# Optimization experiments

Hardware: AMD Instinct MI355X
Metric: run time of the kernel (lower is better)

Reference implementation:

```python
import jax, jax.numpy as jnp
import numpy as np

jax.config.update("jax_enable_x64", True)

# Module hyperparameters (from init_kwargs)
NUM_EMB = 1_000_000
EMB_DIM = 128
COMPRESSION = 1.0 / 64.0
WEIGHT_SIZE = int(NUM_EMB * EMB_DIM * COMPRESSION)  # 2_000_000 (1D compressed table)

# Hash constants matching the CUDA kernel's multiplicative hash:
# hashed_idx = (index * P1 + dim * P2) mod weight_size
P1 = np.uint64(9824516537)
P2 = np.uint64(57857966300227)

BATCH = 16384
BAG_LEN = 50


def _hashed_idx(indices):
    # indices: [N] int -> hashed positions [N, EMB_DIM] into the 1D weight table
    flat = indices.reshape(-1).astype(jnp.uint64)
    dims = jnp.arange(EMB_DIM, dtype=jnp.uint64)
    h = (flat[:, None] * P1 + dims[None, :] * P2) % jnp.uint64(WEIGHT_SIZE)
    return h.astype(jnp.int64)


def setup_inputs() -> dict:
    key = jax.random.key(0)
    k1, k2 = jax.random.split(key)
    indices = jax.random.randint(k1, (BATCH, BAG_LEN), 0, NUM_EMB, dtype=jnp.int64)
    # reset_parameters(): init.normal_(weight)
    weight = jax.random.normal(k2, (WEIGHT_SIZE,), dtype=jnp.float32)
    return {"weight": weight, "indices": indices}


def reference(weight, indices):
    # 2D indices path: each row is one bag of fixed length; mode='sum'.
    B, L = indices.shape
    hidx = _hashed_idx(indices)                      # [B*L, D]
    emb = weight[hidx].reshape(B, L, EMB_DIM)        # gather from compressed table
    return emb.sum(axis=1)                           # [B, D] per-bag sum
```

## Files before the change

kernel.cpp:

```cpp
#include <hip/hip_runtime.h>
#include <stdint.h>


#define WS       2000000
#define EMB_DIM  128
#define BAG_LEN  50
#define BATCH    16384

#define NBLK     256
#define NTHR     1024
#define BAGS_PB  64
#define NQUAD    16
#define QEXT     408
#define RSZE     65536
#define NREG     31
#define SBIG     300227u
#define SENT     0x10000000u

#define GLOAD_LDS16(gp, lp)                                            \
    __builtin_amdgcn_global_load_lds(                                  \
        (const __attribute__((address_space(1))) uint32_t*)(gp),       \
        (__attribute__((address_space(3))) uint32_t*)(lp), 16, 0, 0)

__global__ __launch_bounds__(1024) void conv_bf16(
    const float* __restrict__ w, uint16_t* __restrict__ o)
{
    const int i = (blockIdx.x * 1024 + threadIdx.x) * 4;
    if (i >= WS) return;
    const float4 f = *(const float4*)(w + i);
    uint32_t u0 = __float_as_uint(f.x), u1 = __float_as_uint(f.y);
    uint32_t u2 = __float_as_uint(f.z), u3 = __float_as_uint(f.w);
    ushort4 r;
    r.x = (uint16_t)((u0 + 0x7FFFu + ((u0 >> 16) & 1u)) >> 16);
    r.y = (uint16_t)((u1 + 0x7FFFu + ((u1 >> 16) & 1u)) >> 16);
    r.z = (uint16_t)((u2 + 0x7FFFu + ((u2 >> 16) & 1u)) >> 16);
    r.w = (uint16_t)((u3 + 0x7FFFu + ((u3 >> 16) & 1u)) >> 16);
    *(ushort4*)(o + i) = r;
}

__global__ __launch_bounds__(NTHR, 4) void heb_bf16(
    const uint16_t* __restrict__ wbf,
    const int*      __restrict__ indices,
    float*          __restrict__ out)
{
    __shared__ __align__(16) uint16_t tile[RSZE];
    __shared__ uint32_t extq[NQUAD][QEXT];

    const int tid     = threadIdx.x;
    const int d       = tid & 127;
    const int g       = tid >> 7;
    const int bagBase = blockIdx.x * BAGS_PB;

    uint32_t* araw = (uint32_t*)&tile[0];
    uint32_t* S    = (uint32_t*)&tile[0] + 4096;

    for (int p = tid; p < NQUAD * QEXT; p += NTHR)
        ((uint32_t*)extq)[p] = SENT;
    for (int p = tid; p < BAGS_PB * BAG_LEN; p += NTHR) {
        uint32_t b = (uint32_t)p / 50u;
        uint32_t i = (uint32_t)p - b * 50u;
        uint64_t idx = (uint64_t)(uint32_t)indices[bagBase * BAG_LEN + p];
        araw[b * 52 + i] = (uint32_t)((idx * 9824516537ull) % (uint64_t)WS);
    }
    __syncthreads();

    for (int p = tid; p < BAGS_PB * BAG_LEN; p += NTHR) {
        uint32_t b = (uint32_t)p / 50u;
        uint32_t i = (uint32_t)p - b * 50u;
        uint32_t v = araw[b * 52 + i];
        int rank = 0;
        for (int q = 0; q < BAG_LEN; ++q) {
            uint32_t w = araw[b * 52 + q];
            rank += (w < v || (w == v && q < (int)i)) ? 1 : 0;
        }
        S[b * 52 + rank] = v;
    }
    __syncthreads();

    for (int p = tid; p < BAGS_PB * BAG_LEN; p += NTHR) {
        uint32_t bag = (uint32_t)p / 50u;
        uint32_t i   = (uint32_t)p - bag * 50u;
        uint32_t qd  = bag >> 2, b = bag & 3u;
        uint32_t v = S[bag * 52 + i];
        int r = (int)i;
        for (uint32_t b2 = 0; b2 < 4u; ++b2) {
            if (b2 == b) continue;
            const uint32_t* T = &S[((qd << 2) + b2) * 52];
            uint32_t key = (b2 < b) ? v + 1u : v;
            int lo = 0, hi = 50;
            while (lo < hi) {
                int mid = (lo + hi) >> 1;
                bool lt = T[mid] < key;
                lo = lt ? mid + 1 : lo;
                hi = lt ? hi : mid;
            }
            r += lo;
        }
        extq[qd][r]       = (v << 2) | b;
        extq[qd][r + 200] = ((v + (uint32_t)WS) << 2) | b;
    }
    __syncthreads();

    const uint32_t c  = ((uint32_t)d * SBIG) % (uint32_t)WS;
    const uint32_t C4 = (uint32_t)(((int)c - WS) * 4);
    const uint32_t limit = ((uint32_t)WS - c) << 2;

    uint32_t t4[2], K[2];
    float sm[2][4];
#pragma unroll
    for (int qi = 0; qi < 2; ++qi) {
        const uint32_t* eg = &extq[(g << 1) + qi][0];
        int lo = 0, hi = 200;
        while (lo < hi) {
            int mid = (lo + hi) >> 1;
            bool lt = eg[mid] < limit;
            lo = lt ? mid + 1 : lo;
            hi = lt ? hi : mid;
        }
        t4[qi] = (uint32_t)lo << 2;
        K[qi]  = eg[lo];
        sm[qi][0] = sm[qi][1] = sm[qi][2] = sm[qi][3] = 0.0f;
    }

    for (int r = 0; r < NREG; ++r) {
        const int lo  = r * RSZE;
        const int len = (RSZE < WS - lo) ? RSZE : (WS - lo);
        __syncthreads();

        for (int s = tid; s < (len >> 3); s += NTHR)
            GLOAD_LDS16(wbf + lo + (s << 3), &tile[s << 3]);
        __syncthreads();

        const uint32_t len4 = (uint32_t)len << 2;
        const uint32_t CL   = C4 - (((uint32_t)lo) << 2);
        const char* tb = (const char*)&tile[0];

#pragma unroll
        for (int qi = 0; qi < 2; ++qi) {
            const char* eg = (const char*)&extq[(g << 1) + qi][0];
            uint32_t t_ = t4[qi], K_ = K[qi];
            uint32_t u  = K_ + CL;
            float s0 = sm[qi][0], s1 = sm[qi][1];
            float s2 = sm[qi][2], s3 = sm[qi][3];
            while (u < len4) {
                const uint32_t raw =
                    *(const uint16_t*)(tb + ((u >> 1) & ~1u));
                const float v = __uint_as_float(raw << 16);
                const uint32_t tag = u & 3u;
                s0 += (tag == 0u) ? v : 0.0f;
                s1 += (tag == 1u) ? v : 0.0f;
                s2 += (tag == 2u) ? v : 0.0f;
                s3 += (tag == 3u) ? v : 0.0f;
                t_ += 4u;
                K_  = *(const uint32_t*)(eg + t_);
                u   = K_ + CL;
            }
            t4[qi] = t_; K[qi] = K_;
            sm[qi][0] = s0; sm[qi][1] = s1; sm[qi][2] = s2; sm[qi][3] = s3;
        }
    }

#pragma unroll
    for (int qi = 0; qi < 2; ++qi)
#pragma unroll
        for (int b = 0; b < 4; ++b) {
            const int bag = (g << 3) + (qi << 2) + b;
            out[(size_t)(bagBase + bag) * EMB_DIM + d] = sm[qi][b];
        }
}

#define RSIZE_FB 32768
#define NREG_FB  62
#define EXT_N    104
#define SENT4    0x10000000u

__global__ __launch_bounds__(NTHR, 4) void heb_single(
    const float* __restrict__ weight,
    const int*   __restrict__ indices,
    float*       __restrict__ out)
{
    __shared__ __align__(16) float tile[RSIZE_FB];
    __shared__ uint32_t ext4[BAGS_PB][EXT_N];
    const int tid = threadIdx.x, d = tid & 127, bag_lo = tid >> 7;
    const int bagBase = blockIdx.x * BAGS_PB;
    uint32_t* araw = (uint32_t*)&tile[0];
    for (int p = tid; p < BAGS_PB * BAG_LEN; p += NTHR) {
        uint32_t g = (uint32_t)p / 50u, i = (uint32_t)p - g * 50u;
        uint64_t idx = (uint64_t)(uint32_t)indices[bagBase * BAG_LEN + p];
        araw[g * 52 + i] = (uint32_t)((idx * 9824516537ull) % (uint64_t)WS);
    }
    __syncthreads();
    for (int p = tid; p < BAGS_PB * BAG_LEN; p += NTHR) {
        uint32_t g = (uint32_t)p / 50u, i = (uint32_t)p - g * 50u;
        uint32_t v = araw[g * 52 + i];
        int rank = 0;
        for (int q = 0; q < BAG_LEN; ++q) {
            uint32_t w = araw[g * 52 + q];
            rank += (w < v || (w == v && q < (int)i)) ? 1 : 0;
        }
        ext4[g][rank] = v << 2;
        ext4[g][rank + 50] = (v + (uint32_t)WS) << 2;
    }
    for (int p = tid; p < BAGS_PB * 4; p += NTHR)
        ext4[p >> 2][100 + (p & 3)] = SENT4;
    __syncthreads();
    const uint32_t c = ((uint32_t)d * SBIG) % (uint32_t)WS;
    const uint32_t C4 = (uint32_t)(((int)c - WS) * 4);
    const uint32_t wmc4 = ((uint32_t)WS - c) << 2;
    uint32_t t4[8], h4[8]; float sm[8];
#pragma unroll
    for (int k = 0; k < 8; ++k) {
        const uint32_t* eg = &ext4[(bag_lo << 3) + k][0];
        int nlow = 0;
        for (int q = 0; q < BAG_LEN; ++q) nlow += (eg[q] < wmc4) ? 1 : 0;
        t4[k] = (uint32_t)nlow << 2; h4[k] = eg[nlow] + C4; sm[k] = 0.0f;
    }
    for (int r = 0; r < NREG_FB; ++r) {
        const int lo = r * RSIZE_FB;
        const int len = (RSIZE_FB < WS - lo) ? RSIZE_FB : (WS - lo);
        __syncthreads();
        for (int s = tid; s < (len >> 2); s += NTHR)
            GLOAD_LDS16(weight + lo + (s << 2), &tile[s << 2]);
        __syncthreads();
        const uint32_t lo4 = ((uint32_t)lo) << 2;
        const uint32_t hi4 = (r == NREG_FB - 1) ? (uint32_t)(4 * WS)
                                                : lo4 + ((uint32_t)RSIZE_FB << 2);
        const char* tb = (const char*)&tile[0];
#pragma unroll
        for (int k = 0; k < 8; ++k) {
            const char* eg = (const char*)&ext4[(bag_lo << 3) + k][0];
            uint32_t t_ = t4[k], h_ = h4[k]; float s_ = sm[k];
            while (h_ < hi4) {
                s_ += *(const float*)(tb + (h_ - lo4));
                t_ += 4u;
                h_ = *(const uint32_t*)(eg + t_) + C4;
            }
            t4[k] = t_; h4[k] = h_; sm[k] = s_;
        }
    }
#pragma unroll
    for (int k = 0; k < 8; ++k)
        out[(size_t)(bagBase + (bag_lo << 3) + k) * EMB_DIM + d] = sm[k];
}

extern "C" void kernel_launch(void* const* d_in, const int* in_sizes, int n_in,
                              void* d_out, int out_size, void* d_ws, size_t ws_size,
                              hipStream_t stream)
{
    const float* weight  = (const float*)d_in[0];
    const int*   indices = (const int*)d_in[1];
    float*       out     = (float*)d_out;

    if (ws_size >= (size_t)WS * sizeof(uint16_t)) {
        uint16_t* wbf = (uint16_t*)d_ws;
        conv_bf16<<<(WS / 4 + 1023) / 1024, 1024, 0, stream>>>(weight, wbf);
        heb_bf16<<<NBLK, NTHR, 0, stream>>>(wbf, indices, out);
    } else {
        heb_single<<<NBLK, NTHR, 0, stream>>>(weight, indices, out);
    }
}
```

Before: 227.6 us.

## Merge 8 bags per thread stream and accumulate via LDS atomics

Each thread now walks a single merged sorted list covering 8 bags instead of two 4-bag lists. It accumulates into a shared-memory accumulator with atomicAdd rather than predicated register sums. The LDS tile shrinks to make room for the accumulator, so the number of weight-table regions grows, and the bf16 conversion kernel now processes 8 elements per thread. The aim is to drop the per-element 4-way select-add and the double loop overhead, at the cost of LDS atomics, more region passes and extra barriers.

```diff
diff --git a/kernel.cpp b/kernel.cpp
--- a/kernel.cpp
+++ b/kernel.cpp
@@ -10,41 +10,45 @@
 #define NBLK     256
 #define NTHR     1024
 #define BAGS_PB  64
-#define NQUAD    16
-#define QEXT     408
-#define RSZE     65536
-#define NREG     31
+#define TSZ      49152
+#define NREG     41
 #define SBIG     300227u
-#define SENT     0x10000000u
+#define EXT8_N   808
+#define SENT     0x7FFFFFFFu
 
 #define GLOAD_LDS16(gp, lp)                                            \
     __builtin_amdgcn_global_load_lds(                                  \
         (const __attribute__((address_space(1))) uint32_t*)(gp),       \
         (__attribute__((address_space(3))) uint32_t*)(lp), 16, 0, 0)
 
+__device__ __forceinline__ uint32_t f2bf(float x) {
+    uint32_t u = __float_as_uint(x);
+    return (u + 0x7FFFu + ((u >> 16) & 1u)) >> 16;
+}
+
 __global__ __launch_bounds__(1024) void conv_bf16(
     const float* __restrict__ w, uint16_t* __restrict__ o)
 {
-    const int i = (blockIdx.x * 1024 + threadIdx.x) * 4;
+    const int i = (blockIdx.x * 1024 + threadIdx.x) * 8;
     if (i >= WS) return;
-    const float4 f = *(const float4*)(w + i);
-    uint32_t u0 = __float_as_uint(f.x), u1 = __float_as_uint(f.y);
-    uint32_t u2 = __float_as_uint(f.z), u3 = __float_as_uint(f.w);
-    ushort4 r;
-    r.x = (uint16_t)((u0 + 0x7FFFu + ((u0 >> 16) & 1u)) >> 16);
-    r.y = (uint16_t)((u1 + 0x7FFFu + ((u1 >> 16) & 1u)) >> 16);
-    r.z = (uint16_t)((u2 + 0x7FFFu + ((u2 >> 16) & 1u)) >> 16);
-    r.w = (uint16_t)((u3 + 0x7FFFu + ((u3 >> 16) & 1u)) >> 16);
-    *(ushort4*)(o + i) = r;
-}
-
-__global__ __launch_bounds__(NTHR, 4) void heb_bf16(
+    const float4 f0 = *(const float4*)(w + i);
+    const float4 f1 = *(const float4*)(w + i + 4);
+    uint4 st;
+    st.x = f2bf(f0.x) | (f2bf(f0.y) << 16);
+    st.y = f2bf(f0.z) | (f2bf(f0.w) << 16);
+    st.z = f2bf(f1.x) | (f2bf(f1.y) << 16);
+    st.w = f2bf(f1.z) | (f2bf(f1.w) << 16);
+    *(uint4*)(o + i) = st;
+}
+
+__global__ __launch_bounds__(NTHR, 4) void heb_bf16v2(
     const uint16_t* __restrict__ wbf,
     const int*      __restrict__ indices,
     float*          __restrict__ out)
 {
-    __shared__ __align__(16) uint16_t tile[RSZE];
-    __shared__ uint32_t extq[NQUAD][QEXT];
+    __shared__ __align__(16) uint16_t tile[TSZ];
+    __shared__ float    acc[BAGS_PB * EMB_DIM];
+    __shared__ uint32_t ext8[8][EXT8_N];
 
     const int tid     = threadIdx.x;
     const int d       = tid & 127;
@@ -54,8 +58,9 @@
     uint32_t* araw = (uint32_t*)&tile[0];
     uint32_t* S    = (uint32_t*)&tile[0] + 4096;
 
-    for (int p = tid; p < NQUAD * QEXT; p += NTHR)
-        ((uint32_t*)extq)[p] = SENT;
+    for (int p = tid; p < BAGS_PB * EMB_DIM; p += NTHR) acc[p] = 0.0f;
+    for (int p = tid; p < 8 * EXT8_N; p += NTHR)
+        ((uint32_t*)ext8)[p] = SENT;
     for (int p = tid; p < BAGS_PB * BAG_LEN; p += NTHR) {
         uint32_t b = (uint32_t)p / 50u;
         uint32_t i = (uint32_t)p - b * 50u;
@@ -80,12 +85,12 @@
     for (int p = tid; p < BAGS_PB * BAG_LEN; p += NTHR) {
         uint32_t bag = (uint32_t)p / 50u;
         uint32_t i   = (uint32_t)p - bag * 50u;
-        uint32_t qd  = bag >> 2, b = bag & 3u;
+        uint32_t gg  = bag >> 3, b = bag & 7u;
         uint32_t v = S[bag * 52 + i];
         int r = (int)i;
-        for (uint32_t b2 = 0; b2 < 4u; ++b2) {
+        for (uint32_t b2 = 0; b2 < 8u; ++b2) {
             if (b2 == b) continue;
-            const uint32_t* T = &S[((qd << 2) + b2) * 52];
+            const uint32_t* T = &S[((gg << 3) + b2) * 52];
             uint32_t key = (b2 < b) ? v + 1u : v;
             int lo = 0, hi = 50;
             while (lo < hi) {
@@ -96,77 +101,57 @@
             }
             r += lo;
         }
-        extq[qd][r]       = (v << 2) | b;
-        extq[qd][r + 200] = ((v + (uint32_t)WS) << 2) | b;
+        ext8[gg][r]       = (v << 3) | b;
+        ext8[gg][r + 400] = ((v + (uint32_t)WS) << 3) | b;
     }
     __syncthreads();
 
     const uint32_t c  = ((uint32_t)d * SBIG) % (uint32_t)WS;
-    const uint32_t C4 = (uint32_t)(((int)c - WS) * 4);
-    const uint32_t limit = ((uint32_t)WS - c) << 2;
-
-    uint32_t t4[2], K[2];
-    float sm[2][4];
-#pragma unroll
-    for (int qi = 0; qi < 2; ++qi) {
-        const uint32_t* eg = &extq[(g << 1) + qi][0];
-        int lo = 0, hi = 200;
-        while (lo < hi) {
-            int mid = (lo + hi) >> 1;
-            bool lt = eg[mid] < limit;
-            lo = lt ? mid + 1 : lo;
-            hi = lt ? hi : mid;
-        }
-        t4[qi] = (uint32_t)lo << 2;
-        K[qi]  = eg[lo];
-        sm[qi][0] = sm[qi][1] = sm[qi][2] = sm[qi][3] = 0.0f;
-    }
+    const uint32_t C8 = (uint32_t)(((int)c - WS) * 8);
+    const uint32_t limit = ((uint32_t)WS - c) << 3;
+
+    const uint32_t* eg = &ext8[g][0];
+    int lo_ = 0, hi_ = 400;
+    while (lo_ < hi_) {
+        int mid = (lo_ + hi_) >> 1;
+        bool lt = eg[mid] < limit;
+        lo_ = lt ? mid + 1 : lo_;
+        hi_ = lt ? hi_ : mid;
+    }
+    uint32_t t_ = (uint32_t)lo_ << 2;
+    uint32_t K_ = eg[lo_];
+
+    const char* eb = (const char*)&ext8[g][0];
+    float* accG = acc + (g << 10) + d;
 
     for (int r = 0; r < NREG; ++r) {
-        const int lo  = r * RSZE;
-        const int len = (RSZE < WS - lo) ? RSZE : (WS - lo);
+        const int lo  = r * TSZ;
+        const int len = (TSZ < WS - lo) ? TSZ : (WS - lo);
         __syncthreads();
 
         for (int s = tid; s < (len >> 3); s += NTHR)
             GLOAD_LDS16(wbf + lo + (s << 3), &tile[s << 3]);
         __syncthreads();
 
-        const uint32_t len4 = (uint32_t)len << 2;
-        const uint32_t CL   = C4 - (((uint32_t)lo) << 2);
+        const uint32_t len8 = (uint32_t)len << 3;
+        const uint32_t CL   = C8 - (((uint32_t)lo) << 3);
         const char* tb = (const char*)&tile[0];
 
-#pragma unroll
-        for (int qi = 0; qi < 2; ++qi) {
-            const char* eg = (const char*)&extq[(g << 1) + qi][0];
-            uint32_t t_ = t4[qi], K_ = K[qi];
-            uint32_t u  = K_ + CL;
-            float s0 = sm[qi][0], s1 = sm[qi][1];
-            float s2 = sm[qi][2], s3 = sm[qi][3];
-            while (u < len4) {
-                const uint32_t raw =
-                    *(const uint16_t*)(tb + ((u >> 1) & ~1u));
-                const float v = __uint_as_float(raw << 16);
-                const uint32_t tag = u & 3u;
-                s0 += (tag == 0u) ? v : 0.0f;
-                s1 += (tag == 1u) ? v : 0.0f;
-                s2 += (tag == 2u) ? v : 0.0f;
-                s3 += (tag == 3u) ? v : 0.0f;
-                t_ += 4u;
-                K_  = *(const uint32_t*)(eg + t_);
-                u   = K_ + CL;
-            }
-            t4[qi] = t_; K[qi] = K_;
-            sm[qi][0] = s0; sm[qi][1] = s1; sm[qi][2] = s2; sm[qi][3] = s3;
-        }
-    }
-
-#pragma unroll
-    for (int qi = 0; qi < 2; ++qi)
-#pragma unroll
-        for (int b = 0; b < 4; ++b) {
-            const int bag = (g << 3) + (qi << 2) + b;
-            out[(size_t)(bagBase + bag) * EMB_DIM + d] = sm[qi][b];
-        }
+        uint32_t u = K_ + CL;
+        while (u < len8) {
+            const uint32_t raw =
+                *(const uint16_t*)(tb + ((u >> 2) & ~1u));
+            const float v = __uint_as_float(raw << 16);
+            atomicAdd(accG + ((u & 7u) << 7), v);
+            t_ += 4u;
+            K_  = *(const uint32_t*)(eb + t_);
+            u   = K_ + CL;
+        }
+    }
+    __syncthreads();
+
+    for (int p = tid; p < BAGS_PB * EMB_DIM; p += NTHR)
+        out[(size_t)bagBase * EMB_DIM + p] = acc[p];
 }
 
 #define RSIZE_FB 32768
@@ -253,8 +238,8 @@
 
     if (ws_size >= (size_t)WS * sizeof(uint16_t)) {
         uint16_t* wbf = (uint16_t*)d_ws;
-        conv_bf16<<<(WS / 4 + 1023) / 1024, 1024, 0, stream>>>(weight, wbf);
-        heb_bf16<<<NBLK, NTHR, 0, stream>>>(wbf, indices, out);
+        conv_bf16<<<(WS / 8 + 1023) / 1024, 1024, 0, stream>>>(weight, wbf);
+        heb_bf16v2<<<NBLK, NTHR, 0, stream>>>(wbf, indices, out);
     } else {
         heb_single<<<NBLK, NTHR, 0, stream>>>(weight, indices, out);
     }
```

Measured after the change: 712.0 us. +212.9%, slower.

## Fuse bf16 weight conversion into main kernel via cooperative grid sync

Applied to the files above, without the earlier changes.

The separate fp32-to-bf16 conversion kernel is folded into the main embedding-bag kernel. Each block converts an 8192-element slice of the weight table, then the grid synchronises with a cooperative-groups barrier before the region streaming begins. The conversion now overlaps with the per-block hashing, sorting and binary-search setup, and one kernel launch is removed. In exchange it needs a cooperative launch, whose grid barrier has its own cost and which requires all 256 blocks of 1024 threads to be co-resident.

```diff
diff --git a/kernel.cpp b/kernel.cpp
--- a/kernel.cpp
+++ b/kernel.cpp
@@ -1,5 +1,8 @@
 #include <hip/hip_runtime.h>
+#include <hip/hip_cooperative_groups.h>
 #include <stdint.h>
+
+namespace cg = cooperative_groups;
 
 
 #define WS       2000000
@@ -22,26 +25,16 @@
         (const __attribute__((address_space(1))) uint32_t*)(gp),       \
         (__attribute__((address_space(3))) uint32_t*)(lp), 16, 0, 0)
 
-__global__ __launch_bounds__(1024) void conv_bf16(
-    const float* __restrict__ w, uint16_t* __restrict__ o)
-{
-    const int i = (blockIdx.x * 1024 + threadIdx.x) * 4;
-    if (i >= WS) return;
-    const float4 f = *(const float4*)(w + i);
-    uint32_t u0 = __float_as_uint(f.x), u1 = __float_as_uint(f.y);
-    uint32_t u2 = __float_as_uint(f.z), u3 = __float_as_uint(f.w);
-    ushort4 r;
-    r.x = (uint16_t)((u0 + 0x7FFFu + ((u0 >> 16) & 1u)) >> 16);
-    r.y = (uint16_t)((u1 + 0x7FFFu + ((u1 >> 16) & 1u)) >> 16);
-    r.z = (uint16_t)((u2 + 0x7FFFu + ((u2 >> 16) & 1u)) >> 16);
-    r.w = (uint16_t)((u3 + 0x7FFFu + ((u3 >> 16) & 1u)) >> 16);
-    *(ushort4*)(o + i) = r;
-}
-
-__global__ __launch_bounds__(NTHR, 4) void heb_bf16(
-    const uint16_t* __restrict__ wbf,
-    const int*      __restrict__ indices,
-    float*          __restrict__ out)
+__device__ __forceinline__ uint32_t f2bf(float x) {
+    uint32_t u = __float_as_uint(x);
+    return (u + 0x7FFFu + ((u >> 16) & 1u)) >> 16;
+}
+
+__global__ __launch_bounds__(NTHR, 4) void heb_coop(
+    const float* __restrict__ weight,
+    const int*   __restrict__ indices,
+    float*       __restrict__ out,
+    uint16_t*                 wbf)
 {
     __shared__ __align__(16) uint16_t tile[RSZE];
     __shared__ uint32_t extq[NQUAD][QEXT];
@@ -50,6 +43,20 @@
     const int d       = tid & 127;
     const int g       = tid >> 7;
     const int bagBase = blockIdx.x * BAGS_PB;
+
+    {
+        const int idx = blockIdx.x * 8192 + tid * 8;
+        if (idx < WS) {
+            const float4 f0 = *(const float4*)(weight + idx);
+            const float4 f1 = *(const float4*)(weight + idx + 4);
+            uint4 st;
+            st.x = f2bf(f0.x) | (f2bf(f0.y) << 16);
+            st.y = f2bf(f0.z) | (f2bf(f0.w) << 16);
+            st.z = f2bf(f1.x) | (f2bf(f1.y) << 16);
+            st.w = f2bf(f1.z) | (f2bf(f1.w) << 16);
+            *(uint4*)(wbf + idx) = st;
+        }
+    }
 
     uint32_t* araw = (uint32_t*)&tile[0];
     uint32_t* S    = (uint32_t*)&tile[0] + 4096;
@@ -121,6 +128,9 @@
         K[qi]  = eg[lo];
         sm[qi][0] = sm[qi][1] = sm[qi][2] = sm[qi][3] = 0.0f;
     }
+
+    __threadfence();
+    cg::this_grid().sync();
 
     for (int r = 0; r < NREG; ++r) {
         const int lo  = r * RSZE;
@@ -253,8 +263,9 @@
 
     if (ws_size >= (size_t)WS * sizeof(uint16_t)) {
         uint16_t* wbf = (uint16_t*)d_ws;
-        conv_bf16<<<(WS / 4 + 1023) / 1024, 1024, 0, stream>>>(weight, wbf);
-        heb_bf16<<<NBLK, NTHR, 0, stream>>>(wbf, indices, out);
+        void* args[] = {(void*)&weight, (void*)&indices, (void*)&out, (void*)&wbf};
+        hipLaunchCooperativeKernel((const void*)heb_coop,
+                                   dim3(NBLK), dim3(NTHR), args, 0, stream);
     } else {
         heb_single<<<NBLK, NTHR, 0, stream>>>(weight, indices, out);
     }
```

Result: slower. 338.9 us (+48.9%).
